# Optimization experiments

Hardware: AMD Instinct MI355X
Metric: run time of the kernel (lower is better)

## Reference

```python
import jax, jax.numpy as jnp
import numpy as np

T, HW, C = 64, 24, 1024
MID = 256
WIN = 2  # 'video' forward_type -> 2x2 windows


def setup_inputs() -> dict:
    key = jax.random.key(0)
    k1, k2, k3, k4, k5 = jax.random.split(key, 5)
    return {
        "image_features": jax.random.normal(k1, (T, HW * HW, C), dtype=jnp.float32),
        "Wq": jax.random.normal(k2, (C, MID), dtype=jnp.float32) * 0.02,
        "bq": jax.random.normal(k3, (MID,), dtype=jnp.float32) * 0.02,
        "Wk": jax.random.normal(k4, (C, MID), dtype=jnp.float32) * 0.02,
        "bk": jax.random.normal(k5, (MID,), dtype=jnp.float32) * 0.02,
    }


def reference(image_features, Wq, bq, Wk, bk):
    # forward_type == 'video': 2x2 windowed attention over pooled patches
    t, n, c = image_features.shape
    H = W = int(np.sqrt(n))
    h2, w2 = H // WIN, W // WIN
    # [T, H, W, C] -> [T, h2, 2, w2, 2, C] -> [T, h2, w2, 2, 2, C] -> [T, P, 4, C]
    x = image_features.reshape(t, h2, WIN, w2, WIN, c)
    windows = x.transpose(0, 1, 3, 2, 4, 5).reshape(t, h2 * w2, WIN * WIN, c)
    # avg_pool2d(2,2) == mean over each 2x2 window
    pooled = windows.mean(axis=2)  # [T, P, C]
    q = pooled @ Wq + bq           # [T, P, MID]
    k = windows @ Wk + bk          # [T, P, 4, MID]
    scale = 1.0 / jnp.sqrt(jnp.float32(MID))
    attn = jnp.einsum("tpd,tpwd->tpw", q, k) * scale  # [T, P, 4]
    attn = jnp.nan_to_num(attn)
    attn = jax.nn.softmax(attn, axis=-1)
    attn_feat = jnp.einsum("tpw,tpwc->tpc", attn, windows)  # softmax-weighted value avg
    # query dim has size 1, so .mean(1) in torch is identity here
    return pooled + attn_feat  # [T, P, C]; new_image_size = (h2, w2) is static
```

## Files before the change

kernel.cpp:

```cpp
#include <hip/hip_runtime.h>

#define T_ 64
#define P_ 144
#define NPAIR 9216
#define C_ 1024
#define MID_ 256

typedef __attribute__((ext_vector_type(4))) float f32x4;
typedef __attribute__((ext_vector_type(8))) __bf16 bf16x8;
typedef __attribute__((ext_vector_type(4))) __bf16 bf16x4;

__device__ __forceinline__ void async_copy16(const void* g, void* l) {
  __builtin_amdgcn_global_load_lds(
      (const __attribute__((address_space(1))) unsigned int*)g,
      (__attribute__((address_space(3))) unsigned int*)l, 16, 0, 0);
}

__device__ __forceinline__ int img_row_of(int g) {
  const int pair = g >> 2;
  const int w = g & 3;
  const int t = pair / P_;
  const int pp = pair - t * P_;
  const int wy = pp / 12, wx = pp - wy * 12;
  return t * 576 + 48 * wy + 2 * wx + (w >> 1) * 24 + (w & 1);
}

__global__ void prep_kernel(const float* __restrict__ img,
                            const float* __restrict__ Wq,
                            const float* __restrict__ Wk,
                            __bf16* __restrict__ poolb,
                            __bf16* __restrict__ Wqt,
                            __bf16* __restrict__ Wkt) {
  const int bid = blockIdx.x;
  const int tid = threadIdx.x;
  if (bid < NPAIR) {
    const int t = bid / P_;
    const int p = bid - t * P_;
    const int wy = p / 12, wx = p - wy * 12;
    const int c = tid * 4;
    const float* base = img + ((size_t)t * 576 + 48 * wy + 2 * wx) * C_;
    f32x4 s = *(const f32x4*)(base + c);
    s += *(const f32x4*)(base + (size_t)1 * C_ + c);
    s += *(const f32x4*)(base + (size_t)24 * C_ + c);
    s += *(const f32x4*)(base + (size_t)25 * C_ + c);
    s *= 0.25f;
    bf16x4 pv;
#pragma unroll
    for (int j = 0; j < 4; ++j) pv[j] = (__bf16)s[j];
    *(bf16x4*)(poolb + (size_t)bid * C_ + c) = pv;
  } else {
    __shared__ float tl[32][33];
    const int b = bid - NPAIR;
    const int bx = b & 31;
    const int by = (b >> 5) & 7;
    const int bz = b >> 8;
    const float* src = bz ? Wk : Wq;
    __bf16* dst = bz ? Wkt : Wqt;
    const int tx = tid & 31, ty = tid >> 5;
    const int k0 = bx * 32, n0 = by * 32;
#pragma unroll
    for (int i = 0; i < 32; i += 8)
      tl[ty + i][tx] = src[(size_t)(k0 + ty + i) * MID_ + n0 + tx];
    __syncthreads();
#pragma unroll
    for (int i = 0; i < 32; i += 8)
      dst[(size_t)(n0 + ty + i) * C_ + k0 + tx] = (__bf16)tl[tx][ty + i];
  }
}

__device__ __forceinline__ void mfma_tile(const __bf16* As, const __bf16* Bs,
                                          int wm, int wn, int quad, int lr,
                                          f32x4 acc[4][4]) {
  bf16x8 a[4], b[4];
  const bf16x8* Ap = (const bf16x8*)As;
  const bf16x8* Bp = (const bf16x8*)Bs;
#pragma unroll
  for (int i = 0; i < 4; ++i) {
    a[i] = Ap[(wm * 64 + i * 16 + lr) * 4 + quad];
    b[i] = Bp[(wn * 64 + i * 16 + lr) * 4 + quad];
  }
#pragma unroll
  for (int mi = 0; mi < 4; ++mi)
#pragma unroll
    for (int ni = 0; ni < 4; ++ni)
      acc[mi][ni] = __builtin_amdgcn_mfma_f32_16x16x32_bf16(
          a[mi], b[ni], acc[mi][ni], 0, 0, 0);
}

__global__ __launch_bounds__(256) void gemm_qk_kernel(
    const __bf16* __restrict__ poolb, const float* __restrict__ img,
    const __bf16* __restrict__ Bqt, const __bf16* __restrict__ Bkt,
    const float* __restrict__ bq, const float* __restrict__ bk,
    __bf16* __restrict__ Qb, __bf16* __restrict__ Kb) {
  __shared__ __align__(16) __bf16 As[128 * 32];
  __shared__ __align__(16) __bf16 Bs[128 * 32];
  const int bid = blockIdx.x;
  const bool isQ = bid < 144;
  const __bf16* Bt;
  const float* bias;
  __bf16* Cout;
  int mt, nt;
  if (isQ) {
    Bt = Bqt; bias = bq; Cout = Qb;
    mt = bid >> 1; nt = bid & 1;
  } else {
    const int b = bid - 144;
    Bt = Bkt; bias = bk; Cout = Kb;
    mt = b >> 1; nt = b & 1;
  }
  const int tid = threadIdx.x;
  const int lane = tid & 63;
  const int wv = tid >> 6;
  const int quad = lane >> 4, lr = lane & 15;
  const int wm = wv >> 1, wn = wv & 1;

  const int r0 = tid >> 2, p0 = tid & 3;
  const int wvb = (tid & ~63) * 16;
  const __bf16* gb0 = Bt + ((size_t)nt * 128 + r0) * (size_t)C_ + p0 * 8;
  const __bf16* gb1 = gb0 + (size_t)64 * C_;
  char* BsB0 = (char*)Bs + wvb;
  char* BsB1 = (char*)Bs + 4096 + wvb;

  f32x4 acc[4][4] = {};

  if (isQ) {
    const __bf16* ga0 = poolb + ((size_t)mt * 128 + r0) * (size_t)C_ + p0 * 8;
    const __bf16* ga1 = ga0 + (size_t)64 * C_;
    char* AsB0 = (char*)As + wvb;
    char* AsB1 = (char*)As + 4096 + wvb;
    for (int it = 0; it < 32; ++it) {
      async_copy16(ga0, AsB0);
      async_copy16(ga1, AsB1);
      async_copy16(gb0, BsB0);
      async_copy16(gb1, BsB1);
      ga0 += 32; ga1 += 32; gb0 += 32; gb1 += 32;
      __syncthreads();
      mfma_tile(As, Bs, wm, wn, quad, lr, acc);
      __syncthreads();
    }
  } else {
    const int g0 = mt * 128 + r0;
    const float* fa0 = img + (size_t)img_row_of(g0) * C_ + p0 * 8;
    const float* fa1 = img + (size_t)img_row_of(g0 + 64) * C_ + p0 * 8;
    __bf16* lw0 = As + (size_t)tid * 8;
    __bf16* lw1 = As + (size_t)(tid + 256) * 8;
    for (int it = 0; it < 32; ++it) {
      const f32x4 u0 = *(const f32x4*)fa0;
      const f32x4 u1 = *(const f32x4*)(fa0 + 4);
      const f32x4 u2 = *(const f32x4*)fa1;
      const f32x4 u3 = *(const f32x4*)(fa1 + 4);
      fa0 += 32; fa1 += 32;
      bf16x8 c0, c1;
#pragma unroll
      for (int j = 0; j < 4; ++j) {
        c0[j] = (__bf16)u0[j]; c0[4 + j] = (__bf16)u1[j];
        c1[j] = (__bf16)u2[j]; c1[4 + j] = (__bf16)u3[j];
      }
      *(bf16x8*)lw0 = c0;
      *(bf16x8*)lw1 = c1;
      async_copy16(gb0, BsB0);
      async_copy16(gb1, BsB1);
      gb0 += 32; gb1 += 32;
      __syncthreads();
      mfma_tile(As, Bs, wm, wn, quad, lr, acc);
      __syncthreads();
    }
  }

  const int colb = nt * 128 + wn * 64;
  const int rowb = mt * 128 + wm * 64 + quad * 4;
#pragma unroll
  for (int ni = 0; ni < 4; ++ni) {
    const int col = colb + ni * 16 + lr;
    const float bv = bias[col];
#pragma unroll
    for (int mi = 0; mi < 4; ++mi) {
      const int row = rowb + mi * 16;
#pragma unroll
      for (int r = 0; r < 4; ++r)
        Cout[(size_t)(row + r) * MID_ + col] = (__bf16)(acc[mi][ni][r] + bv);
    }
  }
}

__global__ void attn_out_kernel(const __bf16* __restrict__ Qb,
                                const __bf16* __restrict__ Kb,
                                const float* __restrict__ img,
                                float* __restrict__ out) {
  const int pair = blockIdx.x;
  const int tid = threadIdx.x;
  const int wv = tid >> 6, lane = tid & 63;
  __shared__ float red[4][4];

  const int t = pair / P_;
  const int pp = pair - t * P_;
  const int wy = pp / 12, wx = pp - wy * 12;
  const float* base = img + ((size_t)t * 576 + 48 * wy + 2 * wx) * C_;
  const int c = tid * 4;
  f32x4 v0 = *(const f32x4*)(base + c);
  f32x4 v1 = *(const f32x4*)(base + (size_t)1 * C_ + c);
  f32x4 v2 = *(const f32x4*)(base + (size_t)24 * C_ + c);
  f32x4 v3 = *(const f32x4*)(base + (size_t)25 * C_ + c);

  const float qv = (float)Qb[(size_t)pair * MID_ + tid];
#pragma unroll
  for (int w = 0; w < 4; ++w) {
    float p = qv * (float)Kb[((size_t)pair * 4 + w) * MID_ + tid];
    p += __shfl_down(p, 32);
    p += __shfl_down(p, 16);
    p += __shfl_down(p, 8);
    p += __shfl_down(p, 4);
    p += __shfl_down(p, 2);
    p += __shfl_down(p, 1);
    if (lane == 0) red[w][wv] = p;
  }
  __syncthreads();
  float lg[4];
  float mx = -1e30f;
#pragma unroll
  for (int w = 0; w < 4; ++w) {
    lg[w] = (red[w][0] + red[w][1] + red[w][2] + red[w][3]) * 0.0625f;
    mx = fmaxf(mx, lg[w]);
  }
  float att[4];
  float ssum = 0.f;
#pragma unroll
  for (int w = 0; w < 4; ++w) {
    att[w] = __expf(lg[w] - mx);
    ssum += att[w];
  }
  const float inv = 1.f / ssum;
  const float a0 = att[0] * inv, a1 = att[1] * inv;
  const float a2 = att[2] * inv, a3 = att[3] * inv;

  f32x4 o = (v0 + v1 + v2 + v3) * 0.25f;
  o += a0 * v0 + a1 * v1 + a2 * v2 + a3 * v3;
  *(f32x4*)(out + (size_t)pair * C_ + c) = o;
}

extern "C" void kernel_launch(void* const* d_in, const int* in_sizes, int n_in,
                              void* d_out, int out_size, void* d_ws,
                              size_t ws_size, hipStream_t stream) {
  const float* img = (const float*)d_in[0];
  const float* Wq = (const float*)d_in[1];
  const float* bq = (const float*)d_in[2];
  const float* Wk = (const float*)d_in[3];
  const float* bk = (const float*)d_in[4];
  float* out = (float*)d_out;

  char* ws = (char*)d_ws;
  __bf16* poolb = (__bf16*)ws;
  __bf16* Wqt = (__bf16*)(ws + 18874368);
  __bf16* Wkt = (__bf16*)(ws + 19398656);
  __bf16* Qb = (__bf16*)(ws + 19922944);
  __bf16* Kb = (__bf16*)(ws + 24641536);

  prep_kernel<<<NPAIR + 512, 256, 0, stream>>>(img, Wq, Wk, poolb, Wqt, Wkt);
  gemm_qk_kernel<<<720, 256, 0, stream>>>(poolb, img, Wqt, Wkt, bq, bk, Qb, Kb);
  attn_out_kernel<<<NPAIR, 256, 0, stream>>>(Qb, Kb, img, out);
}
```

Baseline: 315.0 us.

## Fold Wq·Wk^T into a single projection and drop per-window K GEMM

Reassociates the attention logits as pooled·(Wq·Wk^T)·x^T plus a bq·Wk^T term, dropping bk because it adds the same constant to every window logit and softmax ignores that. A small GEMM builds the 1024x1024 combined weight in bf16. A GEMM over the pooled features then produces an fp32 U per window, and the attention kernel dots U with the raw window pixels. This removes the large K projection over all window rows, which read the fp32 image, in exchange for a wider N=1024 GEMM, an fp32 U buffer written and re-read, and extra bf16 rounding in the fused weight.

Measured after the change: 309.0 us. About the same (-1.9%).

```diff
diff --git a/kernel.cpp b/kernel.cpp
--- a/kernel.cpp
+++ b/kernel.cpp
@@ -16,21 +16,14 @@
       (__attribute__((address_space(3))) unsigned int*)l, 16, 0, 0);
 }
 
-__device__ __forceinline__ int img_row_of(int g) {
-  const int pair = g >> 2;
-  const int w = g & 3;
-  const int t = pair / P_;
-  const int pp = pair - t * P_;
-  const int wy = pp / 12, wx = pp - wy * 12;
-  return t * 576 + 48 * wy + 2 * wx + (w >> 1) * 24 + (w & 1);
-}
-
 __global__ void prep_kernel(const float* __restrict__ img,
                             const float* __restrict__ Wq,
+                            const float* __restrict__ bq,
                             const float* __restrict__ Wk,
                             __bf16* __restrict__ poolb,
-                            __bf16* __restrict__ Wqt,
-                            __bf16* __restrict__ Wkt) {
+                            __bf16* __restrict__ Wqb,
+                            __bf16* __restrict__ Wkb,
+                            float* __restrict__ kb) {
   const int bid = blockIdx.x;
   const int tid = threadIdx.x;
   if (bid < NPAIR) {
@@ -48,66 +41,37 @@
 #pragma unroll
     for (int j = 0; j < 4; ++j) pv[j] = (__bf16)s[j];
     *(bf16x4*)(poolb + (size_t)bid * C_ + c) = pv;
+  } else if (bid < NPAIR + 256) {
+    const int c0 = (bid - NPAIR) * 1024 + tid * 4;
+    f32x4 q = *(const f32x4*)(Wq + c0);
+    f32x4 k = *(const f32x4*)(Wk + c0);
+    bf16x4 qb, kbv;
+#pragma unroll
+    for (int j = 0; j < 4; ++j) { qb[j] = (__bf16)q[j]; kbv[j] = (__bf16)k[j]; }
+    *(bf16x4*)(Wqb + c0) = qb;
+    *(bf16x4*)(Wkb + c0) = kbv;
   } else {
-    __shared__ float tl[32][33];
-    const int b = bid - NPAIR;
-    const int bx = b & 31;
-    const int by = (b >> 5) & 7;
-    const int bz = b >> 8;
-    const float* src = bz ? Wk : Wq;
-    __bf16* dst = bz ? Wkt : Wqt;
-    const int tx = tid & 31, ty = tid >> 5;
-    const int k0 = bx * 32, n0 = by * 32;
-#pragma unroll
-    for (int i = 0; i < 32; i += 8)
-      tl[ty + i][tx] = src[(size_t)(k0 + ty + i) * MID_ + n0 + tx];
+    __shared__ float bqs[256];
+    bqs[tid] = bq[tid];
     __syncthreads();
-#pragma unroll
-    for (int i = 0; i < 32; i += 8)
-      dst[(size_t)(n0 + ty + i) * C_ + k0 + tx] = (__bf16)tl[tx][ty + i];
-  }
-}
-
-__device__ __forceinline__ void mfma_tile(const __bf16* As, const __bf16* Bs,
-                                          int wm, int wn, int quad, int lr,
-                                          f32x4 acc[4][4]) {
-  bf16x8 a[4], b[4];
-  const bf16x8* Ap = (const bf16x8*)As;
-  const bf16x8* Bp = (const bf16x8*)Bs;
-#pragma unroll
-  for (int i = 0; i < 4; ++i) {
-    a[i] = Ap[(wm * 64 + i * 16 + lr) * 4 + quad];
-    b[i] = Bp[(wn * 64 + i * 16 + lr) * 4 + quad];
-  }
-#pragma unroll
-  for (int mi = 0; mi < 4; ++mi)
-#pragma unroll
-    for (int ni = 0; ni < 4; ++ni)
-      acc[mi][ni] = __builtin_amdgcn_mfma_f32_16x16x32_bf16(
-          a[mi], b[ni], acc[mi][ni], 0, 0, 0);
-}
-
-__global__ __launch_bounds__(256) void gemm_qk_kernel(
-    const __bf16* __restrict__ poolb, const float* __restrict__ img,
-    const __bf16* __restrict__ Bqt, const __bf16* __restrict__ Bkt,
-    const float* __restrict__ bq, const float* __restrict__ bk,
-    __bf16* __restrict__ Qb, __bf16* __restrict__ Kb) {
+    const int n = (bid - (NPAIR + 256)) * 256 + tid;
+    const float* row = Wk + (size_t)n * MID_;
+    float s = 0.f;
+#pragma unroll 4
+    for (int j = 0; j < 256; ++j) s += row[j] * bqs[j];
+    kb[n] = s;
+  }
+}
+
+template <typename OutT, bool HasBias>
+__global__ __launch_bounds__(256) void gemm_kernel(
+    const __bf16* __restrict__ A, const __bf16* __restrict__ Bt,
+    const float* __restrict__ bias, OutT* __restrict__ C,
+    int K, int ntiles, int ldc) {
   __shared__ __align__(16) __bf16 As[128 * 32];
   __shared__ __align__(16) __bf16 Bs[128 * 32];
   const int bid = blockIdx.x;
-  const bool isQ = bid < 144;
-  const __bf16* Bt;
-  const float* bias;
-  __bf16* Cout;
-  int mt, nt;
-  if (isQ) {
-    Bt = Bqt; bias = bq; Cout = Qb;
-    mt = bid >> 1; nt = bid & 1;
-  } else {
-    const int b = bid - 144;
-    Bt = Bkt; bias = bk; Cout = Kb;
-    mt = b >> 1; nt = b & 1;
-  }
+  const int mt = bid / ntiles, nt = bid - mt * ntiles;
   const int tid = threadIdx.x;
   const int lane = tid & 63;
   const int wv = tid >> 6;
@@ -116,55 +80,41 @@
 
   const int r0 = tid >> 2, p0 = tid & 3;
   const int wvb = (tid & ~63) * 16;
-  const __bf16* gb0 = Bt + ((size_t)nt * 128 + r0) * (size_t)C_ + p0 * 8;
-  const __bf16* gb1 = gb0 + (size_t)64 * C_;
+  const __bf16* ga0 = A + ((size_t)mt * 128 + r0) * (size_t)K + p0 * 8;
+  const __bf16* ga1 = ga0 + (size_t)64 * K;
+  const __bf16* gb0 = Bt + ((size_t)nt * 128 + r0) * (size_t)K + p0 * 8;
+  const __bf16* gb1 = gb0 + (size_t)64 * K;
+  char* AsB0 = (char*)As + wvb;
+  char* AsB1 = (char*)As + 4096 + wvb;
   char* BsB0 = (char*)Bs + wvb;
   char* BsB1 = (char*)Bs + 4096 + wvb;
 
   f32x4 acc[4][4] = {};
-
-  if (isQ) {
-    const __bf16* ga0 = poolb + ((size_t)mt * 128 + r0) * (size_t)C_ + p0 * 8;
-    const __bf16* ga1 = ga0 + (size_t)64 * C_;
-    char* AsB0 = (char*)As + wvb;
-    char* AsB1 = (char*)As + 4096 + wvb;
-    for (int it = 0; it < 32; ++it) {
-      async_copy16(ga0, AsB0);
-      async_copy16(ga1, AsB1);
-      async_copy16(gb0, BsB0);
-      async_copy16(gb1, BsB1);
-      ga0 += 32; ga1 += 32; gb0 += 32; gb1 += 32;
-      __syncthreads();
-      mfma_tile(As, Bs, wm, wn, quad, lr, acc);
-      __syncthreads();
+  const int iters = K >> 5;
+
+  for (int it = 0; it < iters; ++it) {
+    async_copy16(ga0, AsB0);
+    async_copy16(ga1, AsB1);
+    async_copy16(gb0, BsB0);
+    async_copy16(gb1, BsB1);
+    ga0 += 32; ga1 += 32; gb0 += 32; gb1 += 32;
+    __syncthreads();
+
+    bf16x8 a[4], b[4];
+    const bf16x8* Ap = (const bf16x8*)As;
+    const bf16x8* Bp = (const bf16x8*)Bs;
+#pragma unroll
+    for (int i = 0; i < 4; ++i) {
+      a[i] = Ap[(wm * 64 + i * 16 + lr) * 4 + quad];
+      b[i] = Bp[(wn * 64 + i * 16 + lr) * 4 + quad];
     }
-  } else {
-    const int g0 = mt * 128 + r0;
-    const float* fa0 = img + (size_t)img_row_of(g0) * C_ + p0 * 8;
-    const float* fa1 = img + (size_t)img_row_of(g0 + 64) * C_ + p0 * 8;
-    __bf16* lw0 = As + (size_t)tid * 8;
-    __bf16* lw1 = As + (size_t)(tid + 256) * 8;
-    for (int it = 0; it < 32; ++it) {
-      const f32x4 u0 = *(const f32x4*)fa0;
-      const f32x4 u1 = *(const f32x4*)(fa0 + 4);
-      const f32x4 u2 = *(const f32x4*)fa1;
-      const f32x4 u3 = *(const f32x4*)(fa1 + 4);
-      fa0 += 32; fa1 += 32;
-      bf16x8 c0, c1;
-#pragma unroll
-      for (int j = 0; j < 4; ++j) {
-        c0[j] = (__bf16)u0[j]; c0[4 + j] = (__bf16)u1[j];
-        c1[j] = (__bf16)u2[j]; c1[4 + j] = (__bf16)u3[j];
-      }
-      *(bf16x8*)lw0 = c0;
-      *(bf16x8*)lw1 = c1;
-      async_copy16(gb0, BsB0);
-      async_copy16(gb1, BsB1);
-      gb0 += 32; gb1 += 32;
-      __syncthreads();
-      mfma_tile(As, Bs, wm, wn, quad, lr, acc);
-      __syncthreads();
-    }
+#pragma unroll
+    for (int mi = 0; mi < 4; ++mi)
+#pragma unroll
+      for (int ni = 0; ni < 4; ++ni)
+        acc[mi][ni] = __builtin_amdgcn_mfma_f32_16x16x32_bf16(
+            a[mi], b[ni], acc[mi][ni], 0, 0, 0);
+    __syncthreads();
   }
 
   const int colb = nt * 128 + wn * 64;
@@ -172,19 +122,18 @@
 #pragma unroll
   for (int ni = 0; ni < 4; ++ni) {
     const int col = colb + ni * 16 + lr;
-    const float bv = bias[col];
+    const float bv = HasBias ? bias[col] : 0.f;
 #pragma unroll
     for (int mi = 0; mi < 4; ++mi) {
       const int row = rowb + mi * 16;
 #pragma unroll
       for (int r = 0; r < 4; ++r)
-        Cout[(size_t)(row + r) * MID_ + col] = (__bf16)(acc[mi][ni][r] + bv);
+        C[(size_t)(row + r) * ldc + col] = (OutT)(acc[mi][ni][r] + bv);
     }
   }
 }
 
-__global__ void attn_out_kernel(const __bf16* __restrict__ Qb,
-                                const __bf16* __restrict__ Kb,
+__global__ void attn_out_kernel(const float* __restrict__ U,
                                 const float* __restrict__ img,
                                 float* __restrict__ out) {
   const int pair = blockIdx.x;
@@ -201,11 +150,20 @@
   f32x4 v1 = *(const f32x4*)(base + (size_t)1 * C_ + c);
   f32x4 v2 = *(const f32x4*)(base + (size_t)24 * C_ + c);
   f32x4 v3 = *(const f32x4*)(base + (size_t)25 * C_ + c);
-
-  const float qv = (float)Qb[(size_t)pair * MID_ + tid];
+  const f32x4 u4 = *(const f32x4*)(U + (size_t)pair * C_ + c);
+
+  float pd[4];
+#pragma unroll
+  for (int j = 0; j < 4; ++j) {
+  }
+  pd[0] = u4[0] * v0[0] + u4[1] * v0[1] + u4[2] * v0[2] + u4[3] * v0[3];
+  pd[1] = u4[0] * v1[0] + u4[1] * v1[1] + u4[2] * v1[2] + u4[3] * v1[3];
+  pd[2] = u4[0] * v2[0] + u4[1] * v2[1] + u4[2] * v2[2] + u4[3] * v2[3];
+  pd[3] = u4[0] * v3[0] + u4[1] * v3[1] + u4[2] * v3[2] + u4[3] * v3[3];
+
 #pragma unroll
   for (int w = 0; w < 4; ++w) {
-    float p = qv * (float)Kb[((size_t)pair * 4 + w) * MID_ + tid];
+    float p = pd[w];
     p += __shfl_down(p, 32);
     p += __shfl_down(p, 16);
     p += __shfl_down(p, 8);
@@ -246,16 +204,22 @@
   const float* bq = (const float*)d_in[2];
   const float* Wk = (const float*)d_in[3];
   const float* bk = (const float*)d_in[4];
+  (void)bk;
   float* out = (float*)d_out;
 
   char* ws = (char*)d_ws;
   __bf16* poolb = (__bf16*)ws;
-  __bf16* Wqt = (__bf16*)(ws + 18874368);
-  __bf16* Wkt = (__bf16*)(ws + 19398656);
-  __bf16* Qb = (__bf16*)(ws + 19922944);
-  __bf16* Kb = (__bf16*)(ws + 24641536);
-
-  prep_kernel<<<NPAIR + 512, 256, 0, stream>>>(img, Wq, Wk, poolb, Wqt, Wkt);
-  gemm_qk_kernel<<<720, 256, 0, stream>>>(poolb, img, Wqt, Wkt, bq, bk, Qb, Kb);
-  attn_out_kernel<<<NPAIR, 256, 0, stream>>>(Qb, Kb, img, out);
-}
+  __bf16* Wqb = (__bf16*)(ws + 18874368);
+  __bf16* Wkb = (__bf16*)(ws + 19398656);
+  __bf16* H = (__bf16*)(ws + 19922944);
+  float* kb = (float*)(ws + 22020096);
+  float* U = (float*)(ws + 22024192);
+
+  prep_kernel<<<NPAIR + 260, 256, 0, stream>>>(img, Wq, bq, Wk, poolb, Wqb,
+                                               Wkb, kb);
+  gemm_kernel<__bf16, false><<<64, 256, 0, stream>>>(Wkb, Wqb, nullptr, H,
+                                                     MID_, 8, C_);
+  gemm_kernel<float, true><<<576, 256, 0, stream>>>(poolb, H, kb, U, C_, 8,
+                                                    C_);
+  attn_out_kernel<<<NPAIR, 256, 0, stream>>>(U, img, out);
+}
```
